# Kernel optimization log

Measured on AMD Instinct MI355X. Metric: run time of the kernel, lower is better.

Reference implementation:

```python
import jax, jax.numpy as jnp
import numpy as np

N_NODES = 500_000
N_EDGES = 16_000_000
C_IN = 1
C_OUT = 4


def gcn_conv(x, edge_index, W, b):
    """PyG GCNConv: add self-loops, symmetric normalization, linear + scatter-add.
    x: [N, Cin], edge_index: [2, E] (src, dst), W: [Cin, Cout], b: [Cout].
    """
    n = x.shape[0]
    loops = jnp.arange(n, dtype=edge_index.dtype)
    src = jnp.concatenate([edge_index[0], loops])  # [E+N]
    dst = jnp.concatenate([edge_index[1], loops])  # [E+N]
    h = x @ W  # [N, Cout]
    # degree at target nodes (with self-loops)
    deg = jax.ops.segment_sum(jnp.ones_like(dst, dtype=h.dtype), dst, num_segments=n)
    dinv = jnp.where(deg > 0, jax.lax.rsqrt(deg), 0.0)  # deg^{-1/2}
    norm = dinv[src] * dinv[dst]  # [E+N]
    msgs = norm[:, None] * h[src]  # [E+N, Cout] gathered + scaled messages
    out = jax.ops.segment_sum(msgs, dst, num_segments=n)  # scatter-add at targets
    return out + b


def setup_inputs() -> dict:
    key = jax.random.key(0)
    k0, k1, k2, k3 = jax.random.split(key, 4)
    x = jax.random.normal(k0, (N_NODES, C_IN), dtype=jnp.float32)
    edge_index = jax.random.randint(k1, (2, N_EDGES), 0, N_NODES, dtype=jnp.int64)
    W1 = jax.random.normal(k2, (C_IN, C_OUT), dtype=jnp.float32) / np.sqrt(C_IN)
    b1 = jnp.zeros((C_OUT,), dtype=jnp.float32)
    W2 = jax.random.normal(k3, (C_OUT, C_OUT), dtype=jnp.float32) / np.sqrt(C_OUT)
    b2 = jnp.zeros((C_OUT,), dtype=jnp.float32)
    return {"x": x, "edge_index": edge_index, "W1": W1, "b1": b1, "W2": W2, "b2": b2}


def reference(x, edge_index, W1, b1, W2, b2):
    h = jax.nn.relu(gcn_conv(x, edge_index, W1, b1))
    return gcn_conv(h, edge_index, W2, b2)
```

## Files before the change

kernel.cpp:

```cpp
#include <hip/hip_runtime.h>


#define B1_BLOCKS 512
#define B1_THREADS 1024
#define TILE1 16384
#define B2_THREADS 1024
#define TILE2 16384
#define MAXNB1 256
#define SORT_STAGE 12032
#define FB_BLOCKS 512
#define FB_THREADS 1024
#define FB_PAD 8
#define MAXNBF 2048


template <int CTRL, int RM, int KOLD>
__device__ __forceinline__ void seg_step1(int m, float& a) {
  const int mm = __builtin_amdgcn_update_dpp(KOLD, m, CTRL, RM, 0xf, true);
  const float f = (mm == m) ? 1.0f : 0.0f;
  const float ba = __int_as_float(
      __builtin_amdgcn_update_dpp(0, __float_as_int(a), CTRL, RM, 0xf, true));
  a = fmaf(ba, f, a);
}

template <int CTRL, int RM, int KOLD>
__device__ __forceinline__ void seg_step4(int m, float& gx, float& gy,
                                          float& gz, float& gw) {
  const int mm = __builtin_amdgcn_update_dpp(KOLD, m, CTRL, RM, 0xf, true);
  const float f = (mm == m) ? 1.0f : 0.0f;
  const float bx = __int_as_float(
      __builtin_amdgcn_update_dpp(0, __float_as_int(gx), CTRL, RM, 0xf, true));
  const float by = __int_as_float(
      __builtin_amdgcn_update_dpp(0, __float_as_int(gy), CTRL, RM, 0xf, true));
  const float bz = __int_as_float(
      __builtin_amdgcn_update_dpp(0, __float_as_int(gz), CTRL, RM, 0xf, true));
  const float bw = __int_as_float(
      __builtin_amdgcn_update_dpp(0, __float_as_int(gw), CTRL, RM, 0xf, true));
  gx = fmaf(bx, f, gx);
  gy = fmaf(by, f, gy);
  gz = fmaf(bz, f, gz);
  gw = fmaf(bw, f, gw);
}

__device__ __forceinline__ void seg_scan1(int m, float& a) {
  seg_step1<0x111, 0xf, 0>(m, a);
  seg_step1<0x112, 0xf, 0>(m, a);
  seg_step1<0x114, 0xf, 0>(m, a);
// ... 70 lines not shown
      int4 d = reinterpret_cast<const int4*>(dt)[k];
      int4 s = reinterpret_cast<const int4*>(st)[k];
      int r0 = atomicAdd(&wcur[d.x >> 11], 1);
      int r1 = atomicAdd(&wcur[d.y >> 11], 1);
      int r2 = atomicAdd(&wcur[d.z >> 11], 1);
      int r3 = atomicAdd(&wcur[d.w >> 11], 1);
      out[r0] = (s.x << 11) | (d.x & 2047);
      out[r1] = (s.y << 11) | (d.y & 2047);
      out[r2] = (s.z << 11) | (d.z & 2047);
      out[r3] = (s.w << 11) | (d.w & 2047);
    }
    for (int k = (nv << 2) + tid; k < tcnt; k += B1_THREADS) {
      int d = dt[k], s = st[k];
      int r = atomicAdd(&wcur[d >> 11], 1);
      out[r] = (s << 11) | (d & 2047);
    }
    __syncthreads();

    const int wv = tid >> 6, lane = tid & 63;
    for (int j = wv; j < nb1; j += 16) {
      const int c = wcur[j] - toff[j];
      if (!c) continue;
      const int gbase = gb[j];
      const long long pbase = (long long)j * C1;
      for (int q = lane; q < c; q += 64) {
        int gi = gbase + q;
        if (gi < C1) pay1[pbase + gi] = out[toff[j] + q];
      }
    }
    __syncthreads();
  }
}

__global__ __launch_bounds__(B2_THREADS) void k_bin2(
    const int* __restrict__ pay1, const int* __restrict__ gcur1, int C1,
    int C2, int* __restrict__ gcur2, int* __restrict__ pay2) {
  __shared__ int out[TILE2];
  __shared__ int hist[8], toff9[9], wcur[8], gb[8];
  const int cb = blockIdx.x >> 1;
  const int half = blockIdx.x & 1;
  const int tid = threadIdx.x;
  const int Lc = min(gcur1[cb], C1);
  int mid = ((Lc >> 1) + 3) & ~3;
  if (mid > Lc) mid = Lc;
  const int h0 = half ? mid : 0;
  const int h1 = half ? Lc : mid;
  const int* seg = pay1 + (long long)cb * C1;

  for (int tb = h0; tb < h1; tb += TILE2) {
    const int tcnt = min(TILE2, h1 - tb);
    const int nv = tcnt >> 2;
    if (tid < 8) hist[tid] = 0;
    __syncthreads();
    const int* pt = seg + tb;

    for (int k = tid; k < nv; k += B2_THREADS) {
      int4 p = reinterpret_cast<const int4*>(pt)[k];
      atomicAdd(&hist[(p.x >> 8) & 7], 1);
      atomicAdd(&hist[(p.y >> 8) & 7], 1);
      atomicAdd(&hist[(p.z >> 8) & 7], 1);
      atomicAdd(&hist[(p.w >> 8) & 7], 1);
    }
    for (int k = (nv << 2) + tid; k < tcnt; k += B2_THREADS)
      atomicAdd(&hist[(pt[k] >> 8) & 7], 1);
    __syncthreads();

    if (tid == 0) {
      int run = 0;
      for (int j = 0; j < 8; ++j) { toff9[j] = run; run += hist[j]; }
      toff9[8] = run;
    }
    __syncthreads();
    if (tid < 8) {
      wcur[tid] = toff9[tid];
      gb[tid] = hist[tid] ? atomicAdd(&gcur2[cb * 8 + tid], hist[tid]) : 0;
    }
    __syncthreads();

    for (int k = tid; k < nv; k += B2_THREADS) {
      int4 p = reinterpret_cast<const int4*>(pt)[k];
      out[atomicAdd(&wcur[(p.x >> 8) & 7], 1)] = ((p.x >> 11) << 8) | (p.x & 255);
      out[atomicAdd(&wcur[(p.y >> 8) & 7], 1)] = ((p.y >> 11) << 8) | (p.y & 255);
      out[atomicAdd(&wcur[(p.z >> 8) & 7], 1)] = ((p.z >> 11) << 8) | (p.z & 255);
      out[atomicAdd(&wcur[(p.w >> 8) & 7], 1)] = ((p.w >> 11) << 8) | (p.w & 255);
    }
    for (int k = (nv << 2) + tid; k < tcnt; k += B2_THREADS) {
      int p = pt[k];
      out[atomicAdd(&wcur[(p >> 8) & 7], 1)] = ((p >> 11) << 8) | (p & 255);
    }
    __syncthreads();

    const int total = toff9[8];
    for (int q = tid; q < total; q += B2_THREADS) {
      int j = (q >= toff9[4]) ? 4 : 0;
      j += (q >= toff9[j + 2]) ? 2 : 0;
      j += (q >= toff9[j + 1]) ? 1 : 0;
      int o = gb[j] + (q - toff9[j]);
      if (o < C2) pay2[(long long)(cb * 8 + j) * C2 + o] = out[q];
    }
    __syncthreads();
  }
}

__global__ __launch_bounds__(FB_THREADS) void k_bin_flat(
    const int* __restrict__ src, const int* __restrict__ dst, int E,
    int chunk, int nbf, int C, int* __restrict__ gcur,
    int* __restrict__ payload) {
  __shared__ int hist[MAXNBF];
  __shared__ int lbase[MAXNBF];
  const int tid = threadIdx.x;
  const long long e0 = (long long)blockIdx.x * chunk;
  long long rem = (long long)E - e0;
  int lim = rem < 0 ? 0 : (rem < chunk ? (int)rem : chunk);
  for (int j = tid; j < nbf; j += FB_THREADS) hist[j] = 0;
  __syncthreads();
  const int* dch = dst + e0;
  const int* sch = src + e0;
  const int nv = lim >> 2;
  for (int k = tid; k < nv; k += FB_THREADS) {
    int4 d = reinterpret_cast<const int4*>(dch)[k];
    atomicAdd(&hist[d.x >> 8], 1);
    atomicAdd(&hist[d.y >> 8], 1);
    atomicAdd(&hist[d.z >> 8], 1);
    atomicAdd(&hist[d.w >> 8], 1);
  }
  for (int k = (nv << 2) + tid; k < lim; k += FB_THREADS)
    atomicAdd(&hist[dch[k] >> 8], 1);
  __syncthreads();
  for (int j = tid; j < nbf; j += FB_THREADS) {
    int c = hist[j];
    lbase[j] = c ? atomicAdd(&gcur[j], (c + FB_PAD - 1) & ~(FB_PAD - 1)) : 0;
    hist[j] = 0;
  }
  __syncthreads();
  for (int k = tid; k < nv; k += FB_THREADS) {
    int4 d = reinterpret_cast<const int4*>(dch)[k];
    int4 s = reinterpret_cast<const int4*>(sch)[k];
    int b0 = d.x >> 8, b1 = d.y >> 8, b2 = d.z >> 8, b3 = d.w >> 8;
    int r0 = atomicAdd(&hist[b0], 1) + lbase[b0];
    int r1 = atomicAdd(&hist[b1], 1) + lbase[b1];
    int r2 = atomicAdd(&hist[b2], 1) + lbase[b2];
    int r3 = atomicAdd(&hist[b3], 1) + lbase[b3];
    if (r0 < C) payload[(long long)b0 * C + r0] = (s.x << 8) | (d.x & 255);
    if (r1 < C) payload[(long long)b1 * C + r1] = (s.y << 8) | (d.y & 255);
    if (r2 < C) payload[(long long)b2 * C + r2] = (s.z << 8) | (d.z & 255);
    if (r3 < C) payload[(long long)b3 * C + r3] = (s.w << 8) | (d.w & 255);
  }
  for (int k = (nv << 2) + tid; k < lim; k += FB_THREADS) {
    int d = dch[k], s = sch[k];
    int bk = d >> 8;
    int r = atomicAdd(&hist[bk], 1) + lbase[bk];
    if (r < C) payload[(long long)bk * C + r] = (s << 8) | (d & 255);
  }
  __syncthreads();
  for (int j = tid; j < nbf; j += FB_THREADS) {
    int c = hist[j];
    if (c) {
      int pc = (c + FB_PAD - 1) & ~(FB_PAD - 1);
      long long base = (long long)j * C;
      for (int k = lbase[j] + c; k < lbase[j] + pc; ++k)
        if (k < C) payload[base + k] = -1;
    }
  }
}

__global__ __launch_bounds__(256) void k_sort(
    int* __restrict__ payload, const int* __restrict__ gcur, int C,
    int n, const float* __restrict__ x,
    int* __restrict__ off_g, float* __restrict__ y) {
  __shared__ int stage[SORT_STAGE];
  __shared__ int hist[256];
  __shared__ int sbuf[2][256];
  __shared__ int cur[256];
  const int b = blockIdx.x, t = threadIdx.x;
  hist[t] = 0;
  __syncthreads();
  int* seg = payload + (long long)b * C;
  const int L = min(gcur[b], C);
  const int nv = L >> 2;
#pragma unroll 2
  for (int k = t; k < nv; k += 256) {
    int4 p = reinterpret_cast<const int4*>(seg)[k];
    reinterpret_cast<int4*>(stage)[k] = p;
    if (p.x >= 0) atomicAdd(&hist[p.x & 255], 1);
    if (p.y >= 0) atomicAdd(&hist[p.y & 255], 1);
    if (p.z >= 0) atomicAdd(&hist[p.z & 255], 1);
    if (p.w >= 0) atomicAdd(&hist[p.w & 255], 1);
  }
  for (int k = (nv << 2) + t; k < L; k += 256) {
    int p = seg[k];
    stage[k] = p;
    if (p >= 0) atomicAdd(&hist[p & 255], 1);
  }
  __syncthreads();
  sbuf[0][t] = hist[t];
  __syncthreads();
  int pi = 0;
  for (int d = 1; d < 256; d <<= 1) {
    int v = sbuf[pi][t];
    if (t >= d) v += sbuf[pi][t - d];
    sbuf[pi ^ 1][t] = v;
    pi ^= 1;
    __syncthreads();
  }
  const int inc = sbuf[pi][t];
  const int exc = inc - hist[t];
  cur[t] = exc;
  off_g[b * 257 + t] = exc;
  if (t == 255) off_g[b * 257 + 256] = inc;
  const int i = (b << 8) + t;
  if (i < n) y[i] = rsqrtf((float)(hist[t] + 1)) * x[i];
  __syncthreads();
#pragma unroll 4
  for (int k = t; k < L; k += 256) {
    int p = stage[k];
    if (p >= 0) {
      int pos = atomicAdd(&cur[p & 255], 1);
      seg[pos] = p;
    }
  }
}

__global__ __launch_bounds__(256) void k_reduce1(
    const int* __restrict__ payload, const int* __restrict__ off_g, int C,
    int n, const float* __restrict__ y, float2* __restrict__ ds) {
  __shared__ float S[256];
  const int b = blockIdx.x, t = threadIdx.x;
  S[t] = 0.0f;
  __syncthreads();
  const int L = off_g[b * 257 + 256];
  const int* seg = payload + (long long)b * C;
  const int lane = t & 63;
  for (int base = t - lane; base < L; base += 256) {
    int k = base + lane;
    bool valid = k < L;
    int p = 0;
    if (valid) p = __builtin_nontemporal_load(seg + k);
    int m = valid ? (p & 255) : 999;
    float v = valid ? y[p >> 8] : 0.0f;
    seg_scan1(m, v);
    int mn = __shfl_down(m, 1, 64);
    if ((lane == 63 || mn != m) && m < 256) atomicAdd(&S[m], v);
  }
  __syncthreads();
  const int i = (b << 8) + t;
  if (i < n) {
    int deg = off_g[b * 257 + t + 1] - off_g[b * 257 + t];
    float r = rsqrtf((float)(deg + 1));
    ds[i] = make_float2(r, r * (S[t] + y[i]));
  }
}

// ... 32 lines not shown
    float gx = r * (h0 * w2[0] + h1 * w2[4] + h2 * w2[8]  + h3 * w2[12]);
    float gy = r * (h0 * w2[1] + h1 * w2[5] + h2 * w2[9]  + h3 * w2[13]);
    float gz = r * (h0 * w2[2] + h1 * w2[6] + h2 * w2[10] + h3 * w2[14]);
    float gw = r * (h0 * w2[3] + h1 * w2[7] + h2 * w2[11] + h3 * w2[15]);
    seg_scan4(m, gx, gy, gz, gw);
    int mn = __shfl_down(m, 1, 64);
    if ((lane == 63 || mn != m) && m < 256) {
      atomicAdd(&S0[m], gx);
      atomicAdd(&S1[m], gy);
      atomicAdd(&S2[m], gz);
      atomicAdd(&S3[m], gw);
    }
  }
  __syncthreads();
  const int i = (b << 8) + t;
  if (i < n) {
    float2 v = ds[i];
    float r = v.x, s = v.y;
    float h0 = fmaxf(fmaf(s, w10, c10), 0.f);
    float h1 = fmaxf(fmaf(s, w11, c11), 0.f);
    float h2 = fmaxf(fmaf(s, w12, c12), 0.f);
    float h3 = fmaxf(fmaf(s, w13, c13), 0.f);
    float gx = r * (h0 * w2[0] + h1 * w2[4] + h2 * w2[8]  + h3 * w2[12]);
    float gy = r * (h0 * w2[1] + h1 * w2[5] + h2 * w2[9]  + h3 * w2[13]);
    float gz = r * (h0 * w2[2] + h1 * w2[6] + h2 * w2[10] + h3 * w2[14]);
    float gw = r * (h0 * w2[3] + h1 * w2[7] + h2 * w2[11] + h3 * w2[15]);
    out[i] = make_float4(b2[0] + r * (S0[t] + gx),
                         b2[1] + r * (S1[t] + gy),
                         b2[2] + r * (S2[t] + gz),
                         b2[3] + r * (S3[t] + gw));
  }
}

extern "C" void kernel_launch(void* const* d_in, const int* in_sizes, int n_in,
                              void* d_out, int out_size, void* d_ws, size_t ws_size,
                              hipStream_t stream) {
  const float* x  = (const float*)d_in[0];
  const int*   ei = (const int*)d_in[1];
  const float* W1 = (const float*)d_in[2];
  const float* b1 = (const float*)d_in[3];
  const float* W2 = (const float*)d_in[4];
  const float* b2 = (const float*)d_in[5];

  const int n = in_sizes[0];
  const int E = in_sizes[1] / 2;
  const int* src = ei;
  const int* dst = ei + E;

  const int nbf = (n + 255) >> 8;
  const int nb1 = (n + 2047) >> 11;
  auto al = [](size_t v) { return (v + 255) & ~(size_t)255; };

  const size_t nn = (size_t)n;
  size_t sz_off = al((size_t)nbf * 257 * 4);
  size_t sz_y   = al(nn * 4);
  size_t sz_ds  = al(nn * 8);
  size_t sz_gc  = al(((size_t)nb1 + nbf) * 4);
  size_t fixed = sz_off + sz_y + sz_ds + sz_gc;

  long long mean1 = (long long)E / (nb1 > 0 ? nb1 : 1);
  long long C1ll = ((mean1 + 2048 + 1024) + 15) & ~15LL;
  long long mean2 = (long long)E / nbf;
  long long C2ll = ((mean2 + 1024) + 15) & ~15LL;
  size_t need_main = fixed + al((size_t)nb1 * C1ll * 4) + al((size_t)nbf * C2ll * 4);
  const bool main_ok = (n <= 524288) && (nb1 <= MAXNB1) && (nbf <= MAXNBF) &&
                       (C2ll <= SORT_STAGE) && (need_main <= ws_size);

  if (main_ok) {
    const int C1 = (int)C1ll, C2 = (int)C2ll;
    char* p = (char*)d_ws;
    int*    pay1  = (int*)p;    p += al((size_t)nb1 * C1 * 4);
    int*    pay2  = (int*)p;    p += al((size_t)nbf * C2 * 4);
    int*    gcur1 = (int*)p;
    int*    gcur2 = gcur1 + nb1;
    p += sz_gc;
    int*    off_g = (int*)p;    p += sz_off;
    float*  y     = (float*)p;  p += sz_y;
    float2* ds    = (float2*)p; p += sz_ds;

    hipMemsetAsync(gcur1, 0, ((size_t)nb1 + nbf) * 4, stream);

    int chunk = (int)(((long long)E + B1_BLOCKS - 1) / B1_BLOCKS);
    chunk = (chunk + 3) & ~3;

    k_bin1<<<B1_BLOCKS, B1_THREADS, 0, stream>>>(src, dst, E, chunk, nb1, C1,
                                                 gcur1, pay1);
    k_bin2<<<nb1 * 2, B2_THREADS, 0, stream>>>(pay1, gcur1, C1, C2, gcur2,
                                               pay2);
    k_sort<<<nbf, 256, 0, stream>>>(pay2, gcur2, C2, n, x, off_g, y);
    k_reduce1<<<nbf, 256, 0, stream>>>(pay2, off_g, C2, n, y, ds);
    k_reduce2<<<nbf, 256, 0, stream>>>(pay2, off_g, C2, n, ds, W1, b1, W2, b2,
                                       (float4*)d_out);
    return;
  }

  {
    double mean = (double)E / nbf;
    long long Cwant = (long long)(mean * 1.10) +
                      (long long)(FB_BLOCKS * FB_PAD / 2) + 512;
    size_t budget = ws_size > fixed ? ws_size - fixed - 4096 : 0;
    long long Cbud = (long long)(budget / ((size_t)nbf * 4));
    long long Cll = Cwant < Cbud ? Cwant : Cbud;
    if (Cll > SORT_STAGE) Cll = SORT_STAGE;
    int C = (int)(Cll & ~(long long)(FB_PAD - 1));

    char* p = (char*)d_ws;
    int*    pay2  = (int*)p;    p += al((size_t)nbf * C * 4);
    int*    gcur  = (int*)p;    p += sz_gc;
    int*    off_g = (int*)p;    p += sz_off;
    float*  y     = (float*)p;  p += sz_y;
    float2* ds    = (float2*)p; p += sz_ds;

    hipMemsetAsync(gcur, 0, (size_t)nbf * 4, stream);

    int chunk = (int)(((long long)E + FB_BLOCKS - 1) / FB_BLOCKS);
    chunk = (chunk + 3) & ~3;

    k_bin_flat<<<FB_BLOCKS, FB_THREADS, 0, stream>>>(src, dst, E, chunk, nbf,
                                                     C, gcur, pay2);
    k_sort<<<nbf, 256, 0, stream>>>(pay2, gcur, C, n, x, off_g, y);
    k_reduce1<<<nbf, 256, 0, stream>>>(pay2, off_g, C, n, y, ds);
    k_reduce2<<<nbf, 256, 0, stream>>>(pay2, off_g, C, n, ds, W1, b1, W2, b2,
                                       (float4*)d_out);
  }
}
```

Measured before the change: 524.0 us.

## Replace second binning pass and sort with LDS-atomic reductions over coarse bins

Removes the second radix binning pass (k_bin2) and the per-fine-bin sort. Three new kernels (degree count, first-layer reduce, second-layer reduce) work directly on the coarse 2048-node buckets with shared-memory atomics, and each reads the whole bucket payload. This drops one full pass that rewrote the edge payload, plus the sort and offset work. In exchange, the reductions depend on LDS float atomics with possible contention, and only nb1 (~245) blocks of 1024 threads run, which may leave the GPU underfilled. Float summation order also becomes nondeterministic.

```diff
diff --git a/kernel.cpp b/kernel.cpp
--- a/kernel.cpp
+++ b/kernel.cpp
@@ -1,18 +1,17 @@
 #include <hip/hip_runtime.h>
 
+
+typedef int iv4 __attribute__((ext_vector_type(4)));
 
 #define B1_BLOCKS 512
 #define B1_THREADS 1024
 #define TILE1 16384
-#define B2_THREADS 1024
-#define TILE2 16384
 #define MAXNB1 256
 #define SORT_STAGE 12032
 #define FB_BLOCKS 512
 #define FB_THREADS 1024
 #define FB_PAD 8
 #define MAXNBF 2048
-
 
 template <int CTRL, int RM, int KOLD>
 __device__ __forceinline__ void seg_step1(int m, float& a) {
@@ -149,73 +148,159 @@
   }
 }
 
-__global__ __launch_bounds__(B2_THREADS) void k_bin2(
+__global__ __launch_bounds__(1024) void k_cnt(
     const int* __restrict__ pay1, const int* __restrict__ gcur1, int C1,
-    int C2, int* __restrict__ gcur2, int* __restrict__ pay2) {
-  __shared__ int out[TILE2];
-  __shared__ int hist[8], toff9[9], wcur[8], gb[8];
-  const int cb = blockIdx.x >> 1;
-  const int half = blockIdx.x & 1;
-  const int tid = threadIdx.x;
-  const int Lc = min(gcur1[cb], C1);
-  int mid = ((Lc >> 1) + 3) & ~3;
-  if (mid > Lc) mid = Lc;
-  const int h0 = half ? mid : 0;
-  const int h1 = half ? Lc : mid;
-  const int* seg = pay1 + (long long)cb * C1;
-
-  for (int tb = h0; tb < h1; tb += TILE2) {
-    const int tcnt = min(TILE2, h1 - tb);
-    const int nv = tcnt >> 2;
-    if (tid < 8) hist[tid] = 0;
-    __syncthreads();
-    const int* pt = seg + tb;
-
-    for (int k = tid; k < nv; k += B2_THREADS) {
-      int4 p = reinterpret_cast<const int4*>(pt)[k];
-      atomicAdd(&hist[(p.x >> 8) & 7], 1);
-      atomicAdd(&hist[(p.y >> 8) & 7], 1);
-      atomicAdd(&hist[(p.z >> 8) & 7], 1);
-      atomicAdd(&hist[(p.w >> 8) & 7], 1);
-    }
-    for (int k = (nv << 2) + tid; k < tcnt; k += B2_THREADS)
-      atomicAdd(&hist[(pt[k] >> 8) & 7], 1);
-    __syncthreads();
-
-    if (tid == 0) {
-      int run = 0;
-      for (int j = 0; j < 8; ++j) { toff9[j] = run; run += hist[j]; }
-      toff9[8] = run;
-    }
-    __syncthreads();
-    if (tid < 8) {
-      wcur[tid] = toff9[tid];
-      gb[tid] = hist[tid] ? atomicAdd(&gcur2[cb * 8 + tid], hist[tid]) : 0;
-    }
-    __syncthreads();
-
-    for (int k = tid; k < nv; k += B2_THREADS) {
-      int4 p = reinterpret_cast<const int4*>(pt)[k];
-      out[atomicAdd(&wcur[(p.x >> 8) & 7], 1)] = ((p.x >> 11) << 8) | (p.x & 255);
-      out[atomicAdd(&wcur[(p.y >> 8) & 7], 1)] = ((p.y >> 11) << 8) | (p.y & 255);
-      out[atomicAdd(&wcur[(p.z >> 8) & 7], 1)] = ((p.z >> 11) << 8) | (p.z & 255);
-      out[atomicAdd(&wcur[(p.w >> 8) & 7], 1)] = ((p.w >> 11) << 8) | (p.w & 255);
-    }
-    for (int k = (nv << 2) + tid; k < tcnt; k += B2_THREADS) {
-      int p = pt[k];
-      out[atomicAdd(&wcur[(p >> 8) & 7], 1)] = ((p >> 11) << 8) | (p & 255);
-    }
-    __syncthreads();
-
-    const int total = toff9[8];
-    for (int q = tid; q < total; q += B2_THREADS) {
-      int j = (q >= toff9[4]) ? 4 : 0;
-      j += (q >= toff9[j + 2]) ? 2 : 0;
-      j += (q >= toff9[j + 1]) ? 1 : 0;
-      int o = gb[j] + (q - toff9[j]);
-      if (o < C2) pay2[(long long)(cb * 8 + j) * C2 + o] = out[q];
-    }
-    __syncthreads();
+    int n, const float* __restrict__ x, int* __restrict__ deg_g,
+    float* __restrict__ y) {
+  __shared__ int hist[2048];
+  const int b = blockIdx.x, t = threadIdx.x;
+  hist[t] = 0;
+  hist[t + 1024] = 0;
+  __syncthreads();
+  const int L = min(gcur1[b], C1);
+  const int* seg = pay1 + (long long)b * C1;
+  const int nv = L >> 2;
+  for (int k = t; k < nv; k += 1024) {
+    iv4 p = __builtin_nontemporal_load(reinterpret_cast<const iv4*>(seg) + k);
+    atomicAdd(&hist[p.x & 2047], 1);
+    atomicAdd(&hist[p.y & 2047], 1);
+    atomicAdd(&hist[p.z & 2047], 1);
+    atomicAdd(&hist[p.w & 2047], 1);
+  }
+  for (int k = (nv << 2) + t; k < L; k += 1024) {
+    int p = __builtin_nontemporal_load(seg + k);
+    atomicAdd(&hist[p & 2047], 1);
+  }
+  __syncthreads();
+  const int base = b << 11;
+#pragma unroll
+  for (int q = 0; q < 2; ++q) {
+    const int sl = t + q * 1024;
+    const int i = base + sl;
+    if (i < n) {
+      const int d = hist[sl];
+      deg_g[i] = d;
+      y[i] = rsqrtf((float)(d + 1)) * x[i];
+    }
+  }
+}
+
+__global__ __launch_bounds__(1024) void k_red1c(
+    const int* __restrict__ pay1, const int* __restrict__ gcur1, int C1,
+    int n, const float* __restrict__ y, const int* __restrict__ deg_g,
+    float2* __restrict__ ds) {
+  __shared__ float S[2048];
+  const int b = blockIdx.x, t = threadIdx.x;
+  S[t] = 0.0f;
+  S[t + 1024] = 0.0f;
+  __syncthreads();
+  const int L = min(gcur1[b], C1);
+  const int* seg = pay1 + (long long)b * C1;
+  const int nv = L >> 2;
+  for (int k = t; k < nv; k += 1024) {
+    iv4 p = __builtin_nontemporal_load(reinterpret_cast<const iv4*>(seg) + k);
+    float vx = y[p.x >> 11];
+    float vy = y[p.y >> 11];
+    float vz = y[p.z >> 11];
+    float vw = y[p.w >> 11];
+    atomicAdd(&S[p.x & 2047], vx);
+    atomicAdd(&S[p.y & 2047], vy);
+    atomicAdd(&S[p.z & 2047], vz);
+    atomicAdd(&S[p.w & 2047], vw);
+  }
+  for (int k = (nv << 2) + t; k < L; k += 1024) {
+    int p = __builtin_nontemporal_load(seg + k);
+    atomicAdd(&S[p & 2047], y[p >> 11]);
+  }
+  __syncthreads();
+  const int base = b << 11;
+#pragma unroll
+  for (int q = 0; q < 2; ++q) {
+    const int sl = t + q * 1024;
+    const int i = base + sl;
+    if (i < n) {
+      const float r = rsqrtf((float)(deg_g[i] + 1));
+      ds[i] = make_float2(r, r * (S[sl] + y[i]));
+    }
+  }
+}
+
+__global__ __launch_bounds__(1024) void k_red2c(
+    const int* __restrict__ pay1, const int* __restrict__ gcur1, int C1,
+    int n, const float2* __restrict__ ds,
+    const float* __restrict__ W1, const float* __restrict__ b1,
+    const float* __restrict__ W2, const float* __restrict__ b2,
+    float4* __restrict__ out) {
+  __shared__ float S0[2048], S1[2048], S2[2048], S3[2048];
+  const int b = blockIdx.x, t = threadIdx.x;
+  S0[t] = 0.f; S0[t + 1024] = 0.f;
+  S1[t] = 0.f; S1[t + 1024] = 0.f;
+  S2[t] = 0.f; S2[t + 1024] = 0.f;
+  S3[t] = 0.f; S3[t + 1024] = 0.f;
+  __syncthreads();
+  const float w10 = W1[0], w11 = W1[1], w12 = W1[2], w13 = W1[3];
+  const float c10 = b1[0], c11 = b1[1], c12 = b1[2], c13 = b1[3];
+  float w2[16];
+#pragma unroll
+  for (int k = 0; k < 16; ++k) w2[k] = W2[k];
+
+  const int L = min(gcur1[b], C1);
+  const int* seg = pay1 + (long long)b * C1;
+  const int nv = L >> 2;
+  for (int k = t; k < nv; k += 1024) {
+    iv4 p4 = __builtin_nontemporal_load(reinterpret_cast<const iv4*>(seg) + k);
+#pragma unroll
+    for (int c = 0; c < 4; ++c) {
+      const int p = (c == 0) ? p4.x : (c == 1) ? p4.y : (c == 2) ? p4.z : p4.w;
+      const int m = p & 2047;
+      const float2 v = ds[p >> 11];
+      const float r = v.x, s = v.y;
+      const float h0 = fmaxf(fmaf(s, w10, c10), 0.f);
+      const float h1 = fmaxf(fmaf(s, w11, c11), 0.f);
+      const float h2 = fmaxf(fmaf(s, w12, c12), 0.f);
+      const float h3 = fmaxf(fmaf(s, w13, c13), 0.f);
+      atomicAdd(&S0[m], r * (h0 * w2[0] + h1 * w2[4] + h2 * w2[8]  + h3 * w2[12]));
+      atomicAdd(&S1[m], r * (h0 * w2[1] + h1 * w2[5] + h2 * w2[9]  + h3 * w2[13]));
+      atomicAdd(&S2[m], r * (h0 * w2[2] + h1 * w2[6] + h2 * w2[10] + h3 * w2[14]));
+      atomicAdd(&S3[m], r * (h0 * w2[3] + h1 * w2[7] + h2 * w2[11] + h3 * w2[15]));
+    }
+  }
+  for (int k = (nv << 2) + t; k < L; k += 1024) {
+    const int p = __builtin_nontemporal_load(seg + k);
+    const int m = p & 2047;
+    const float2 v = ds[p >> 11];
+    const float r = v.x, s = v.y;
+    const float h0 = fmaxf(fmaf(s, w10, c10), 0.f);
+    const float h1 = fmaxf(fmaf(s, w11, c11), 0.f);
+    const float h2 = fmaxf(fmaf(s, w12, c12), 0.f);
+    const float h3 = fmaxf(fmaf(s, w13, c13), 0.f);
+    atomicAdd(&S0[m], r * (h0 * w2[0] + h1 * w2[4] + h2 * w2[8]  + h3 * w2[12]));
+    atomicAdd(&S1[m], r * (h0 * w2[1] + h1 * w2[5] + h2 * w2[9]  + h3 * w2[13]));
+    atomicAdd(&S2[m], r * (h0 * w2[2] + h1 * w2[6] + h2 * w2[10] + h3 * w2[14]));
+    atomicAdd(&S3[m], r * (h0 * w2[3] + h1 * w2[7] + h2 * w2[11] + h3 * w2[15]));
+  }
+  __syncthreads();
+  const int base = b << 11;
+#pragma unroll
+  for (int q = 0; q < 2; ++q) {
+    const int sl = t + q * 1024;
+    const int i = base + sl;
+    if (i < n) {
+      const float2 v = ds[i];
+      const float r = v.x, s = v.y;
+      const float h0 = fmaxf(fmaf(s, w10, c10), 0.f);
+      const float h1 = fmaxf(fmaf(s, w11, c11), 0.f);
+      const float h2 = fmaxf(fmaf(s, w12, c12), 0.f);
+      const float h3 = fmaxf(fmaf(s, w13, c13), 0.f);
+      const float sx = r * (h0 * w2[0] + h1 * w2[4] + h2 * w2[8]  + h3 * w2[12]);
+      const float sy = r * (h0 * w2[1] + h1 * w2[5] + h2 * w2[9]  + h3 * w2[13]);
+      const float sz = r * (h0 * w2[2] + h1 * w2[6] + h2 * w2[10] + h3 * w2[14]);
+      const float sw = r * (h0 * w2[3] + h1 * w2[7] + h2 * w2[11] + h3 * w2[15]);
+      out[i] = make_float4(b2[0] + r * (S0[sl] + sx),
+                           b2[1] + r * (S1[sl] + sy),
+                           b2[2] + r * (S2[sl] + sz),
+                           b2[3] + r * (S3[sl] + sw));
+    }
   }
 }
 
@@ -453,49 +538,44 @@
   auto al = [](size_t v) { return (v + 255) & ~(size_t)255; };
 
   const size_t nn = (size_t)n;
-  size_t sz_off = al((size_t)nbf * 257 * 4);
   size_t sz_y   = al(nn * 4);
+  size_t sz_deg = al(nn * 4);
   size_t sz_ds  = al(nn * 8);
-  size_t sz_gc  = al(((size_t)nb1 + nbf) * 4);
-  size_t fixed = sz_off + sz_y + sz_ds + sz_gc;
 
   long long mean1 = (long long)E / (nb1 > 0 ? nb1 : 1);
-  long long C1ll = ((mean1 + 2048 + 1024) + 15) & ~15LL;
-  long long mean2 = (long long)E / nbf;
-  long long C2ll = ((mean2 + 1024) + 15) & ~15LL;
-  size_t need_main = fixed + al((size_t)nb1 * C1ll * 4) + al((size_t)nbf * C2ll * 4);
-  const bool main_ok = (n <= 524288) && (nb1 <= MAXNB1) && (nbf <= MAXNBF) &&
-                       (C2ll <= SORT_STAGE) && (need_main <= ws_size);
+  long long C1ll = ((mean1 + 3072) + 15) & ~15LL;
+  size_t need_main = al((size_t)nb1 * C1ll * 4) + al((size_t)nb1 * 4) +
+                     sz_y + sz_deg + sz_ds;
+  const bool main_ok = (n <= 524288) && (nb1 <= MAXNB1) &&
+                       (need_main <= ws_size);
 
   if (main_ok) {
-    const int C1 = (int)C1ll, C2 = (int)C2ll;
+    const int C1 = (int)C1ll;
     char* p = (char*)d_ws;
     int*    pay1  = (int*)p;    p += al((size_t)nb1 * C1 * 4);
-    int*    pay2  = (int*)p;    p += al((size_t)nbf * C2 * 4);
-    int*    gcur1 = (int*)p;
-    int*    gcur2 = gcur1 + nb1;
-    p += sz_gc;
-    int*    off_g = (int*)p;    p += sz_off;
+    int*    gcur1 = (int*)p;    p += al((size_t)nb1 * 4);
+    int*    deg_g = (int*)p;    p += sz_deg;
     float*  y     = (float*)p;  p += sz_y;
     float2* ds    = (float2*)p; p += sz_ds;
 
-    hipMemsetAsync(gcur1, 0, ((size_t)nb1 + nbf) * 4, stream);
+    hipMemsetAsync(gcur1, 0, (size_t)nb1 * 4, stream);
 
     int chunk = (int)(((long long)E + B1_BLOCKS - 1) / B1_BLOCKS);
     chunk = (chunk + 3) & ~3;
 
     k_bin1<<<B1_BLOCKS, B1_THREADS, 0, stream>>>(src, dst, E, chunk, nb1, C1,
                                                  gcur1, pay1);
-    k_bin2<<<nb1 * 2, B2_THREADS, 0, stream>>>(pay1, gcur1, C1, C2, gcur2,
-                                               pay2);
-    k_sort<<<nbf, 256, 0, stream>>>(pay2, gcur2, C2, n, x, off_g, y);
-    k_reduce1<<<nbf, 256, 0, stream>>>(pay2, off_g, C2, n, y, ds);
-    k_reduce2<<<nbf, 256, 0, stream>>>(pay2, off_g, C2, n, ds, W1, b1, W2, b2,
-                                       (float4*)d_out);
+    k_cnt<<<nb1, 1024, 0, stream>>>(pay1, gcur1, C1, n, x, deg_g, y);
+    k_red1c<<<nb1, 1024, 0, stream>>>(pay1, gcur1, C1, n, y, deg_g, ds);
+    k_red2c<<<nb1, 1024, 0, stream>>>(pay1, gcur1, C1, n, ds, W1, b1, W2, b2,
+                                      (float4*)d_out);
     return;
   }
 
   {
+    size_t sz_off = al((size_t)nbf * 257 * 4);
+    size_t sz_gc  = al((size_t)nbf * 4);
+    size_t fixed = sz_off + sz_y + sz_ds + sz_gc;
     double mean = (double)E / nbf;
     long long Cwant = (long long)(mean * 1.10) +
                       (long long)(FB_BLOCKS * FB_PAD / 2) + 512;
```

Measured after the change: 677.0 us. 1.29x slower.

## Replace per-bucket sort with degree histogram and shared-atomic unsorted reductions

Applied to the files above, without the earlier changes.

Removes the k_sort pass, which sorted each 256-node bucket by destination. Node degrees are now counted in a shared-memory histogram inside the second binning kernel and flushed with global atomics. A tiny kernel computes y = rsqrt(deg+1)*x, and both reduction passes read the unsorted bucket payload and accumulate into 256-entry shared arrays with atomicAdd. This trades a sort pass and its offset table for shared-memory atomic contention and nondeterministic float summation order. The memset also grows to cover the degree array.

```diff
diff --git a/kernel.cpp b/kernel.cpp
--- a/kernel.cpp
+++ b/kernel.cpp
@@ -12,7 +12,6 @@
 #define FB_THREADS 1024
 #define FB_PAD 8
 #define MAXNBF 2048
-
 
 template <int CTRL, int RM, int KOLD>
 __device__ __forceinline__ void seg_step1(int m, float& a) {
@@ -149,10 +148,12 @@
   }
 }
 
-__global__ __launch_bounds__(B2_THREADS) void k_bin2(
+__global__ __launch_bounds__(B2_THREADS) void k_bin2d(
     const int* __restrict__ pay1, const int* __restrict__ gcur1, int C1,
-    int C2, int* __restrict__ gcur2, int* __restrict__ pay2) {
+    int C2, int* __restrict__ gcur2, int* __restrict__ pay2,
+    int n, int* __restrict__ deg_g) {
   __shared__ int out[TILE2];
+  __shared__ int dh[2048];
   __shared__ int hist[8], toff9[9], wcur[8], gb[8];
   const int cb = blockIdx.x >> 1;
   const int half = blockIdx.x & 1;
@@ -164,6 +165,10 @@
   const int h1 = half ? Lc : mid;
   const int* seg = pay1 + (long long)cb * C1;
 
+  dh[tid] = 0;
+  dh[tid + 1024] = 0;
+  __syncthreads();
+
   for (int tb = h0; tb < h1; tb += TILE2) {
     const int tcnt = min(TILE2, h1 - tb);
     const int nv = tcnt >> 2;
@@ -177,9 +182,16 @@
       atomicAdd(&hist[(p.y >> 8) & 7], 1);
       atomicAdd(&hist[(p.z >> 8) & 7], 1);
       atomicAdd(&hist[(p.w >> 8) & 7], 1);
-    }
-    for (int k = (nv << 2) + tid; k < tcnt; k += B2_THREADS)
-      atomicAdd(&hist[(pt[k] >> 8) & 7], 1);
+      atomicAdd(&dh[p.x & 2047], 1);
+      atomicAdd(&dh[p.y & 2047], 1);
+      atomicAdd(&dh[p.z & 2047], 1);
+      atomicAdd(&dh[p.w & 2047], 1);
+    }
+    for (int k = (nv << 2) + tid; k < tcnt; k += B2_THREADS) {
+      int p = pt[k];
+      atomicAdd(&hist[(p >> 8) & 7], 1);
+      atomicAdd(&dh[p & 2047], 1);
+    }
     __syncthreads();
 
     if (tid == 0) {
@@ -216,6 +228,96 @@
       if (o < C2) pay2[(long long)(cb * 8 + j) * C2 + o] = out[q];
     }
     __syncthreads();
+  }
+
+  const int nbase = cb << 11;
+#pragma unroll
+  for (int q = 0; q < 2; ++q) {
+    const int j = tid + q * 1024;
+    const int c = dh[j];
+    const int i = nbase + j;
+    if (c && i < n) atomicAdd(&deg_g[i], c);
+  }
+}
+
+__global__ __launch_bounds__(256) void k_y(
+    int n, const int* __restrict__ deg_g, const float* __restrict__ x,
+    float* __restrict__ y) {
+  const int i = blockIdx.x * 256 + threadIdx.x;
+  if (i < n) y[i] = rsqrtf((float)(deg_g[i] + 1)) * x[i];
+}
+
+__global__ __launch_bounds__(256) void k_red1u(
+    const int* __restrict__ pay2, const int* __restrict__ gcur2, int C2,
+    int n, const float* __restrict__ y, const int* __restrict__ deg_g,
+    float2* __restrict__ ds) {
+  __shared__ float S[256];
+  const int b = blockIdx.x, t = threadIdx.x;
+  S[t] = 0.0f;
+  __syncthreads();
+  const int L = min(gcur2[b], C2);
+  const int* seg = pay2 + (long long)b * C2;
+  for (int k = t; k < L; k += 256) {
+    const int p = __builtin_nontemporal_load(seg + k);
+    atomicAdd(&S[p & 255], y[p >> 8]);
+  }
+  __syncthreads();
+  const int i = (b << 8) + t;
+  if (i < n) {
+    const float r = rsqrtf((float)(deg_g[i] + 1));
+    ds[i] = make_float2(r, r * (S[t] + y[i]));
+  }
+}
+
+__global__ __launch_bounds__(256) void k_red2u(
+    const int* __restrict__ pay2, const int* __restrict__ gcur2, int C2,
+    int n, const float2* __restrict__ ds,
+    const float* __restrict__ W1, const float* __restrict__ b1,
+    const float* __restrict__ W2, const float* __restrict__ b2,
+    float4* __restrict__ out) {
+  __shared__ float S0[256], S1[256], S2[256], S3[256];
+  const int b = blockIdx.x, t = threadIdx.x;
+  S0[t] = 0.f; S1[t] = 0.f; S2[t] = 0.f; S3[t] = 0.f;
+  __syncthreads();
+  const float w10 = W1[0], w11 = W1[1], w12 = W1[2], w13 = W1[3];
+  const float c10 = b1[0], c11 = b1[1], c12 = b1[2], c13 = b1[3];
+  float w2[16];
+#pragma unroll
+  for (int k = 0; k < 16; ++k) w2[k] = W2[k];
+
+  const int L = min(gcur2[b], C2);
+  const int* seg = pay2 + (long long)b * C2;
+  for (int k = t; k < L; k += 256) {
+    const int p = __builtin_nontemporal_load(seg + k);
+    const int m = p & 255;
+    const float2 v = ds[p >> 8];
+    const float r = v.x, s = v.y;
+    const float h0 = fmaxf(fmaf(s, w10, c10), 0.f);
+    const float h1 = fmaxf(fmaf(s, w11, c11), 0.f);
+    const float h2 = fmaxf(fmaf(s, w12, c12), 0.f);
+    const float h3 = fmaxf(fmaf(s, w13, c13), 0.f);
+    atomicAdd(&S0[m], r * (h0 * w2[0] + h1 * w2[4] + h2 * w2[8]  + h3 * w2[12]));
+    atomicAdd(&S1[m], r * (h0 * w2[1] + h1 * w2[5] + h2 * w2[9]  + h3 * w2[13]));
+    atomicAdd(&S2[m], r * (h0 * w2[2] + h1 * w2[6] + h2 * w2[10] + h3 * w2[14]));
+    atomicAdd(&S3[m], r * (h0 * w2[3] + h1 * w2[7] + h2 * w2[11] + h3 * w2[15]));
+  }
+  __syncthreads();
+  const int i = (b << 8) + t;
+  if (i < n) {
+    const float2 v = ds[i];
+    const float r = v.x, s = v.y;
+    const float h0 = fmaxf(fmaf(s, w10, c10), 0.f);
+    const float h1 = fmaxf(fmaf(s, w11, c11), 0.f);
+    const float h2 = fmaxf(fmaf(s, w12, c12), 0.f);
+    const float h3 = fmaxf(fmaf(s, w13, c13), 0.f);
+    const float sx = r * (h0 * w2[0] + h1 * w2[4] + h2 * w2[8]  + h3 * w2[12]);
+    const float sy = r * (h0 * w2[1] + h1 * w2[5] + h2 * w2[9]  + h3 * w2[13]);
+    const float sz = r * (h0 * w2[2] + h1 * w2[6] + h2 * w2[10] + h3 * w2[14]);
+    const float sw = r * (h0 * w2[3] + h1 * w2[7] + h2 * w2[11] + h3 * w2[15]);
+    out[i] = make_float4(b2[0] + r * (S0[t] + sx),
+                         b2[1] + r * (S1[t] + sy),
+                         b2[2] + r * (S2[t] + sz),
+                         b2[3] + r * (S3[t] + sw));
   }
 }
 
@@ -453,19 +555,18 @@
   auto al = [](size_t v) { return (v + 255) & ~(size_t)255; };
 
   const size_t nn = (size_t)n;
-  size_t sz_off = al((size_t)nbf * 257 * 4);
   size_t sz_y   = al(nn * 4);
   size_t sz_ds  = al(nn * 8);
-  size_t sz_gc  = al(((size_t)nb1 + nbf) * 4);
-  size_t fixed = sz_off + sz_y + sz_ds + sz_gc;
 
   long long mean1 = (long long)E / (nb1 > 0 ? nb1 : 1);
   long long C1ll = ((mean1 + 2048 + 1024) + 15) & ~15LL;
-  long long mean2 = (long long)E / nbf;
+  long long mean2 = (long long)E / (nbf > 0 ? nbf : 1);
   long long C2ll = ((mean2 + 1024) + 15) & ~15LL;
-  size_t need_main = fixed + al((size_t)nb1 * C1ll * 4) + al((size_t)nbf * C2ll * 4);
-  const bool main_ok = (n <= 524288) && (nb1 <= MAXNB1) && (nbf <= MAXNBF) &&
-                       (C2ll <= SORT_STAGE) && (need_main <= ws_size);
+  size_t sz_zero = al(((size_t)nb1 + nbf + nn) * 4);
+  size_t need_main = al((size_t)nb1 * C1ll * 4) + al((size_t)nbf * C2ll * 4) +
+                     sz_zero + sz_y + sz_ds;
+  const bool main_ok = (n <= 524288) && (nb1 <= MAXNB1) &&
+                       (need_main <= ws_size);
 
   if (main_ok) {
     const int C1 = (int)C1ll, C2 = (int)C2ll;
@@ -474,28 +575,31 @@
     int*    pay2  = (int*)p;    p += al((size_t)nbf * C2 * 4);
     int*    gcur1 = (int*)p;
     int*    gcur2 = gcur1 + nb1;
-    p += sz_gc;
-    int*    off_g = (int*)p;    p += sz_off;
+    int*    deg_g = gcur2 + nbf;
+    p += sz_zero;
     float*  y     = (float*)p;  p += sz_y;
     float2* ds    = (float2*)p; p += sz_ds;
 
-    hipMemsetAsync(gcur1, 0, ((size_t)nb1 + nbf) * 4, stream);
+    hipMemsetAsync(gcur1, 0, ((size_t)nb1 + nbf + nn) * 4, stream);
 
     int chunk = (int)(((long long)E + B1_BLOCKS - 1) / B1_BLOCKS);
     chunk = (chunk + 3) & ~3;
 
     k_bin1<<<B1_BLOCKS, B1_THREADS, 0, stream>>>(src, dst, E, chunk, nb1, C1,
                                                  gcur1, pay1);
-    k_bin2<<<nb1 * 2, B2_THREADS, 0, stream>>>(pay1, gcur1, C1, C2, gcur2,
-                                               pay2);
-    k_sort<<<nbf, 256, 0, stream>>>(pay2, gcur2, C2, n, x, off_g, y);
-    k_reduce1<<<nbf, 256, 0, stream>>>(pay2, off_g, C2, n, y, ds);
-    k_reduce2<<<nbf, 256, 0, stream>>>(pay2, off_g, C2, n, ds, W1, b1, W2, b2,
-                                       (float4*)d_out);
+    k_bin2d<<<nb1 * 2, B2_THREADS, 0, stream>>>(pay1, gcur1, C1, C2, gcur2,
+                                                pay2, n, deg_g);
+    k_y<<<(n + 255) / 256, 256, 0, stream>>>(n, deg_g, x, y);
+    k_red1u<<<nbf, 256, 0, stream>>>(pay2, gcur2, C2, n, y, deg_g, ds);
+    k_red2u<<<nbf, 256, 0, stream>>>(pay2, gcur2, C2, n, ds, W1, b1, W2, b2,
+                                     (float4*)d_out);
     return;
   }
 
   {
+    size_t sz_off = al((size_t)nbf * 257 * 4);
+    size_t sz_gc  = al((size_t)nbf * 4);
+    size_t fixed = sz_off + sz_y + sz_ds + sz_gc;
     double mean = (double)E / nbf;
     long long Cwant = (long long)(mean * 1.10) +
                       (long long)(FB_BLOCKS * FB_PAD / 2) + 512;
```

Measured after the change: 705.2 us. +34.6%, slower.

## Fuse second binning pass and per-bucket sort into one counting-sort kernel

Applied to the files above, without the earlier changes.

Replaces the k_bin2 (split coarse buckets into 8 sub-buckets) and k_sort (in-place 256-way counting sort per fine bucket) kernels with a single k_csort kernel. Each 1024-thread block takes one coarse bucket of 2048 nodes, builds a 2048-entry histogram in shared memory, prefix-scans it, writes the degree-based y and the off_g offsets, then scatters entries directly into their final sorted positions in pay2. This removes one full read/write pass over the edge payload and one kernel launch, along with the gcur2 counters. In exchange the final scatter goes to global memory through 2048 shared atomic cursors with less locality, and only 256 large blocks run, which may limit occupancy.

```diff
diff --git a/kernel.cpp b/kernel.cpp
--- a/kernel.cpp
+++ b/kernel.cpp
@@ -4,15 +4,12 @@
 #define B1_BLOCKS 512
 #define B1_THREADS 1024
 #define TILE1 16384
-#define B2_THREADS 1024
-#define TILE2 16384
 #define MAXNB1 256
 #define SORT_STAGE 12032
 #define FB_BLOCKS 512
 #define FB_THREADS 1024
 #define FB_PAD 8
 #define MAXNBF 2048
-
 
 template <int CTRL, int RM, int KOLD>
 __device__ __forceinline__ void seg_step1(int m, float& a) {
@@ -149,192 +146,78 @@
   }
 }
 
-__global__ __launch_bounds__(B2_THREADS) void k_bin2(
+__global__ __launch_bounds__(1024) void k_csort(
     const int* __restrict__ pay1, const int* __restrict__ gcur1, int C1,
-    int C2, int* __restrict__ gcur2, int* __restrict__ pay2) {
-  __shared__ int out[TILE2];
-  __shared__ int hist[8], toff9[9], wcur[8], gb[8];
-  const int cb = blockIdx.x >> 1;
-  const int half = blockIdx.x & 1;
-  const int tid = threadIdx.x;
-  const int Lc = min(gcur1[cb], C1);
-  int mid = ((Lc >> 1) + 3) & ~3;
-  if (mid > Lc) mid = Lc;
-  const int h0 = half ? mid : 0;
-  const int h1 = half ? Lc : mid;
-  const int* seg = pay1 + (long long)cb * C1;
-
-  for (int tb = h0; tb < h1; tb += TILE2) {
-    const int tcnt = min(TILE2, h1 - tb);
-    const int nv = tcnt >> 2;
-    if (tid < 8) hist[tid] = 0;
-    __syncthreads();
-    const int* pt = seg + tb;
-
-    for (int k = tid; k < nv; k += B2_THREADS) {
-      int4 p = reinterpret_cast<const int4*>(pt)[k];
-      atomicAdd(&hist[(p.x >> 8) & 7], 1);
-      atomicAdd(&hist[(p.y >> 8) & 7], 1);
-      atomicAdd(&hist[(p.z >> 8) & 7], 1);
-      atomicAdd(&hist[(p.w >> 8) & 7], 1);
-    }
-    for (int k = (nv << 2) + tid; k < tcnt; k += B2_THREADS)
-      atomicAdd(&hist[(pt[k] >> 8) & 7], 1);
-    __syncthreads();
-
-    if (tid == 0) {
-      int run = 0;
-      for (int j = 0; j < 8; ++j) { toff9[j] = run; run += hist[j]; }
-      toff9[8] = run;
-    }
-    __syncthreads();
-    if (tid < 8) {
-      wcur[tid] = toff9[tid];
-      gb[tid] = hist[tid] ? atomicAdd(&gcur2[cb * 8 + tid], hist[tid]) : 0;
-    }
-    __syncthreads();
-
-    for (int k = tid; k < nv; k += B2_THREADS) {
-      int4 p = reinterpret_cast<const int4*>(pt)[k];
-      out[atomicAdd(&wcur[(p.x >> 8) & 7], 1)] = ((p.x >> 11) << 8) | (p.x & 255);
-      out[atomicAdd(&wcur[(p.y >> 8) & 7], 1)] = ((p.y >> 11) << 8) | (p.y & 255);
-      out[atomicAdd(&wcur[(p.z >> 8) & 7], 1)] = ((p.z >> 11) << 8) | (p.z & 255);
-      out[atomicAdd(&wcur[(p.w >> 8) & 7], 1)] = ((p.w >> 11) << 8) | (p.w & 255);
-    }
-    for (int k = (nv << 2) + tid; k < tcnt; k += B2_THREADS) {
-      int p = pt[k];
-      out[atomicAdd(&wcur[(p >> 8) & 7], 1)] = ((p >> 11) << 8) | (p & 255);
-    }
-    __syncthreads();
-
-    const int total = toff9[8];
-    for (int q = tid; q < total; q += B2_THREADS) {
-      int j = (q >= toff9[4]) ? 4 : 0;
-      j += (q >= toff9[j + 2]) ? 2 : 0;
-      j += (q >= toff9[j + 1]) ? 1 : 0;
-      int o = gb[j] + (q - toff9[j]);
-      if (o < C2) pay2[(long long)(cb * 8 + j) * C2 + o] = out[q];
-    }
-    __syncthreads();
-  }
-}
-
-__global__ __launch_bounds__(FB_THREADS) void k_bin_flat(
-    const int* __restrict__ src, const int* __restrict__ dst, int E,
-    int chunk, int nbf, int C, int* __restrict__ gcur,
-    int* __restrict__ payload) {
-  __shared__ int hist[MAXNBF];
-  __shared__ int lbase[MAXNBF];
-  const int tid = threadIdx.x;
-  const long long e0 = (long long)blockIdx.x * chunk;
-  long long rem = (long long)E - e0;
-  int lim = rem < 0 ? 0 : (rem < chunk ? (int)rem : chunk);
-  for (int j = tid; j < nbf; j += FB_THREADS) hist[j] = 0;
-  __syncthreads();
-  const int* dch = dst + e0;
-  const int* sch = src + e0;
-  const int nv = lim >> 2;
-  for (int k = tid; k < nv; k += FB_THREADS) {
-    int4 d = reinterpret_cast<const int4*>(dch)[k];
-    atomicAdd(&hist[d.x >> 8], 1);
-    atomicAdd(&hist[d.y >> 8], 1);
-    atomicAdd(&hist[d.z >> 8], 1);
-    atomicAdd(&hist[d.w >> 8], 1);
-  }
-  for (int k = (nv << 2) + tid; k < lim; k += FB_THREADS)
-    atomicAdd(&hist[dch[k] >> 8], 1);
-  __syncthreads();
-  for (int j = tid; j < nbf; j += FB_THREADS) {
-    int c = hist[j];
-    lbase[j] = c ? atomicAdd(&gcur[j], (c + FB_PAD - 1) & ~(FB_PAD - 1)) : 0;
-    hist[j] = 0;
-  }
-  __syncthreads();
-  for (int k = tid; k < nv; k += FB_THREADS) {
-    int4 d = reinterpret_cast<const int4*>(dch)[k];
-    int4 s = reinterpret_cast<const int4*>(sch)[k];
-    int b0 = d.x >> 8, b1 = d.y >> 8, b2 = d.z >> 8, b3 = d.w >> 8;
-    int r0 = atomicAdd(&hist[b0], 1) + lbase[b0];
-    int r1 = atomicAdd(&hist[b1], 1) + lbase[b1];
-    int r2 = atomicAdd(&hist[b2], 1) + lbase[b2];
-    int r3 = atomicAdd(&hist[b3], 1) + lbase[b3];
-    if (r0 < C) payload[(long long)b0 * C + r0] = (s.x << 8) | (d.x & 255);
-    if (r1 < C) payload[(long long)b1 * C + r1] = (s.y << 8) | (d.y & 255);
-    if (r2 < C) payload[(long long)b2 * C + r2] = (s.z << 8) | (d.z & 255);
-    if (r3 < C) payload[(long long)b3 * C + r3] = (s.w << 8) | (d.w & 255);
-  }
-  for (int k = (nv << 2) + tid; k < lim; k += FB_THREADS) {
-    int d = dch[k], s = sch[k];
-    int bk = d >> 8;
-    int r = atomicAdd(&hist[bk], 1) + lbase[bk];
-    if (r < C) payload[(long long)bk * C + r] = (s << 8) | (d & 255);
-  }
-  __syncthreads();
-  for (int j = tid; j < nbf; j += FB_THREADS) {
-    int c = hist[j];
-    if (c) {
-      int pc = (c + FB_PAD - 1) & ~(FB_PAD - 1);
-      long long base = (long long)j * C;
-      for (int k = lbase[j] + c; k < lbase[j] + pc; ++k)
-        if (k < C) payload[base + k] = -1;
-    }
-  }
-}
-
-__global__ __launch_bounds__(256) void k_sort(
-    int* __restrict__ payload, const int* __restrict__ gcur, int C,
-    int n, const float* __restrict__ x,
-    int* __restrict__ off_g, float* __restrict__ y) {
-  __shared__ int stage[SORT_STAGE];
-  __shared__ int hist[256];
-  __shared__ int sbuf[2][256];
-  __shared__ int cur[256];
+    int C2, int n, const float* __restrict__ x,
+    int* __restrict__ off_g, float* __restrict__ y,
+    int* __restrict__ pay2) {
+  __shared__ int dh[2048];
+  __shared__ int off2[2048];
+  __shared__ int sb[2][1024];
   const int b = blockIdx.x, t = threadIdx.x;
-  hist[t] = 0;
-  __syncthreads();
-  int* seg = payload + (long long)b * C;
-  const int L = min(gcur[b], C);
+  const int L = min(gcur1[b], C1);
+  const int* seg = pay1 + (long long)b * C1;
+  dh[t] = 0;
+  dh[t + 1024] = 0;
+  __syncthreads();
+
   const int nv = L >> 2;
-#pragma unroll 2
-  for (int k = t; k < nv; k += 256) {
+  for (int k = t; k < nv; k += 1024) {
     int4 p = reinterpret_cast<const int4*>(seg)[k];
-    reinterpret_cast<int4*>(stage)[k] = p;
-    if (p.x >= 0) atomicAdd(&hist[p.x & 255], 1);
-    if (p.y >= 0) atomicAdd(&hist[p.y & 255], 1);
-    if (p.z >= 0) atomicAdd(&hist[p.z & 255], 1);
-    if (p.w >= 0) atomicAdd(&hist[p.w & 255], 1);
-  }
-  for (int k = (nv << 2) + t; k < L; k += 256) {
-    int p = seg[k];
-    stage[k] = p;
-    if (p >= 0) atomicAdd(&hist[p & 255], 1);
-  }
-  __syncthreads();
-  sbuf[0][t] = hist[t];
-  __syncthreads();
-  int pi = 0;
-  for (int d = 1; d < 256; d <<= 1) {
-    int v = sbuf[pi][t];
-    if (t >= d) v += sbuf[pi][t - d];
-    sbuf[pi ^ 1][t] = v;
-    pi ^= 1;
-    __syncthreads();
-  }
-  const int inc = sbuf[pi][t];
-  const int exc = inc - hist[t];
-  cur[t] = exc;
-  off_g[b * 257 + t] = exc;
-  if (t == 255) off_g[b * 257 + 256] = inc;
-  const int i = (b << 8) + t;
-  if (i < n) y[i] = rsqrtf((float)(hist[t] + 1)) * x[i];
-  __syncthreads();
-#pragma unroll 4
-  for (int k = t; k < L; k += 256) {
-    int p = stage[k];
-    if (p >= 0) {
-      int pos = atomicAdd(&cur[p & 255], 1);
-      seg[pos] = p;
-    }
+    atomicAdd(&dh[p.x & 2047], 1);
+    atomicAdd(&dh[p.y & 2047], 1);
+    atomicAdd(&dh[p.z & 2047], 1);
+    atomicAdd(&dh[p.w & 2047], 1);
+  }
+  for (int k = (nv << 2) + t; k < L; k += 1024)
+    atomicAdd(&dh[seg[k] & 2047], 1);
+  __syncthreads();
+
+#pragma unroll
+  for (int r = 0; r < 2; ++r) {
+    const int base = r << 10;
+    const int c0 = dh[base + t];
+    sb[0][t] = c0;
+    __syncthreads();
+    int pi = 0;
+    for (int d = 1; d < 256; d <<= 1) {
+      int v = sb[pi][t];
+      if ((t & 255) >= d) v += sb[pi][t - d];
+      sb[pi ^ 1][t] = v;
+      pi ^= 1;
+      __syncthreads();
+    }
+    const int inc = sb[pi][t];
+    const int exc = inc - c0;
+    off2[base + t] = exc;
+    const int f = (b << 3) + ((base + t) >> 8);
+    const int tt = t & 255;
+    off_g[f * 257 + tt] = min(exc, C2);
+    if (tt == 255) off_g[f * 257 + 256] = min(inc, C2);
+    const int i = (b << 11) + base + t;
+    if (i < n) y[i] = rsqrtf((float)(c0 + 1)) * x[i];
+    __syncthreads();
+  }
+
+  for (int k = t; k < nv; k += 1024) {
+    int4 p = reinterpret_cast<const int4*>(seg)[k];
+#pragma unroll
+    for (int c = 0; c < 4; ++c) {
+      const int pv = (c == 0) ? p.x : (c == 1) ? p.y : (c == 2) ? p.z : p.w;
+      const int j = pv & 2047;
+      const int pos = atomicAdd(&off2[j], 1);
+      if (pos < C2)
+        pay2[(long long)((b << 3) + (j >> 8)) * C2 + pos] =
+            ((pv >> 11) << 8) | (j & 255);
+    }
+  }
+  for (int k = (nv << 2) + t; k < L; k += 1024) {
+    const int pv = seg[k];
+    const int j = pv & 2047;
+    const int pos = atomicAdd(&off2[j], 1);
+    if (pos < C2)
+      pay2[(long long)((b << 3) + (j >> 8)) * C2 + pos] =
+          ((pv >> 11) << 8) | (j & 255);
   }
 }
 
@@ -433,6 +316,125 @@
   }
 }
 
+__global__ __launch_bounds__(FB_THREADS) void k_bin_flat(
+    const int* __restrict__ src, const int* __restrict__ dst, int E,
+    int chunk, int nbf, int C, int* __restrict__ gcur,
+    int* __restrict__ payload) {
+  __shared__ int hist[MAXNBF];
+  __shared__ int lbase[MAXNBF];
+  const int tid = threadIdx.x;
+  const long long e0 = (long long)blockIdx.x * chunk;
+  long long rem = (long long)E - e0;
+  int lim = rem < 0 ? 0 : (rem < chunk ? (int)rem : chunk);
+  for (int j = tid; j < nbf; j += FB_THREADS) hist[j] = 0;
+  __syncthreads();
+  const int* dch = dst + e0;
+  const int* sch = src + e0;
+  const int nv = lim >> 2;
+  for (int k = tid; k < nv; k += FB_THREADS) {
+    int4 d = reinterpret_cast<const int4*>(dch)[k];
+    atomicAdd(&hist[d.x >> 8], 1);
+    atomicAdd(&hist[d.y >> 8], 1);
+    atomicAdd(&hist[d.z >> 8], 1);
+    atomicAdd(&hist[d.w >> 8], 1);
+  }
+  for (int k = (nv << 2) + tid; k < lim; k += FB_THREADS)
+    atomicAdd(&hist[dch[k] >> 8], 1);
+  __syncthreads();
+  for (int j = tid; j < nbf; j += FB_THREADS) {
+    int c = hist[j];
+    lbase[j] = c ? atomicAdd(&gcur[j], (c + FB_PAD - 1) & ~(FB_PAD - 1)) : 0;
+    hist[j] = 0;
+  }
+  __syncthreads();
+  for (int k = tid; k < nv; k += FB_THREADS) {
+    int4 d = reinterpret_cast<const int4*>(dch)[k];
+    int4 s = reinterpret_cast<const int4*>(sch)[k];
+    int b0 = d.x >> 8, b1 = d.y >> 8, b2 = d.z >> 8, b3 = d.w >> 8;
+    int r0 = atomicAdd(&hist[b0], 1) + lbase[b0];
+    int r1 = atomicAdd(&hist[b1], 1) + lbase[b1];
+    int r2 = atomicAdd(&hist[b2], 1) + lbase[b2];
+    int r3 = atomicAdd(&hist[b3], 1) + lbase[b3];
+    if (r0 < C) payload[(long long)b0 * C + r0] = (s.x << 8) | (d.x & 255);
+    if (r1 < C) payload[(long long)b1 * C + r1] = (s.y << 8) | (d.y & 255);
+    if (r2 < C) payload[(long long)b2 * C + r2] = (s.z << 8) | (d.z & 255);
+    if (r3 < C) payload[(long long)b3 * C + r3] = (s.w << 8) | (d.w & 255);
+  }
+  for (int k = (nv << 2) + tid; k < lim; k += FB_THREADS) {
+    int d = dch[k], s = sch[k];
+    int bk = d >> 8;
+    int r = atomicAdd(&hist[bk], 1) + lbase[bk];
+    if (r < C) payload[(long long)bk * C + r] = (s << 8) | (d & 255);
+  }
+  __syncthreads();
+  for (int j = tid; j < nbf; j += FB_THREADS) {
+    int c = hist[j];
+    if (c) {
+      int pc = (c + FB_PAD - 1) & ~(FB_PAD - 1);
+      long long base = (long long)j * C;
+      for (int k = lbase[j] + c; k < lbase[j] + pc; ++k)
+        if (k < C) payload[base + k] = -1;
+    }
+  }
+}
+
+__global__ __launch_bounds__(256) void k_sort(
+    int* __restrict__ payload, const int* __restrict__ gcur, int C,
+    int n, const float* __restrict__ x,
+    int* __restrict__ off_g, float* __restrict__ y) {
+  __shared__ int stage[SORT_STAGE];
+  __shared__ int hist[256];
+  __shared__ int sbuf[2][256];
+  __shared__ int cur[256];
+  const int b = blockIdx.x, t = threadIdx.x;
+  hist[t] = 0;
+  __syncthreads();
+  int* seg = payload + (long long)b * C;
+  const int L = min(gcur[b], C);
+  const int nv = L >> 2;
+#pragma unroll 2
+  for (int k = t; k < nv; k += 256) {
+    int4 p = reinterpret_cast<const int4*>(seg)[k];
+    reinterpret_cast<int4*>(stage)[k] = p;
+    if (p.x >= 0) atomicAdd(&hist[p.x & 255], 1);
+    if (p.y >= 0) atomicAdd(&hist[p.y & 255], 1);
+    if (p.z >= 0) atomicAdd(&hist[p.z & 255], 1);
+    if (p.w >= 0) atomicAdd(&hist[p.w & 255], 1);
+  }
+  for (int k = (nv << 2) + t; k < L; k += 256) {
+    int p = seg[k];
+    stage[k] = p;
+    if (p >= 0) atomicAdd(&hist[p & 255], 1);
+  }
+  __syncthreads();
+  sbuf[0][t] = hist[t];
+  __syncthreads();
+  int pi = 0;
+  for (int d = 1; d < 256; d <<= 1) {
+    int v = sbuf[pi][t];
+    if (t >= d) v += sbuf[pi][t - d];
+    sbuf[pi ^ 1][t] = v;
+    pi ^= 1;
+    __syncthreads();
+  }
+  const int inc = sbuf[pi][t];
+  const int exc = inc - hist[t];
+  cur[t] = exc;
+  off_g[b * 257 + t] = exc;
+  if (t == 255) off_g[b * 257 + 256] = inc;
+  const int i = (b << 8) + t;
+  if (i < n) y[i] = rsqrtf((float)(hist[t] + 1)) * x[i];
+  __syncthreads();
+#pragma unroll 4
+  for (int k = t; k < L; k += 256) {
+    int p = stage[k];
+    if (p >= 0) {
+      int pos = atomicAdd(&cur[p & 255], 1);
+      seg[pos] = p;
+    }
+  }
+}
+
 extern "C" void kernel_launch(void* const* d_in, const int* in_sizes, int n_in,
                               void* d_out, int out_size, void* d_ws, size_t ws_size,
                               hipStream_t stream) {
@@ -456,39 +458,35 @@
   size_t sz_off = al((size_t)nbf * 257 * 4);
   size_t sz_y   = al(nn * 4);
   size_t sz_ds  = al(nn * 8);
-  size_t sz_gc  = al(((size_t)nb1 + nbf) * 4);
-  size_t fixed = sz_off + sz_y + sz_ds + sz_gc;
 
   long long mean1 = (long long)E / (nb1 > 0 ? nb1 : 1);
   long long C1ll = ((mean1 + 2048 + 1024) + 15) & ~15LL;
-  long long mean2 = (long long)E / nbf;
+  long long mean2 = (long long)E / (nbf > 0 ? nbf : 1);
   long long C2ll = ((mean2 + 1024) + 15) & ~15LL;
-  size_t need_main = fixed + al((size_t)nb1 * C1ll * 4) + al((size_t)nbf * C2ll * 4);
-  const bool main_ok = (n <= 524288) && (nb1 <= MAXNB1) && (nbf <= MAXNBF) &&
-                       (C2ll <= SORT_STAGE) && (need_main <= ws_size);
+  size_t need_main = al((size_t)nb1 * C1ll * 4) + al((size_t)nbf * C2ll * 4) +
+                     al((size_t)nb1 * 4) + sz_off + sz_y + sz_ds;
+  const bool main_ok = (n <= 524288) && (nb1 <= MAXNB1) &&
+                       ((nb1 << 3) >= nbf) && (need_main <= ws_size);
 
   if (main_ok) {
     const int C1 = (int)C1ll, C2 = (int)C2ll;
     char* p = (char*)d_ws;
     int*    pay1  = (int*)p;    p += al((size_t)nb1 * C1 * 4);
     int*    pay2  = (int*)p;    p += al((size_t)nbf * C2 * 4);
-    int*    gcur1 = (int*)p;
-    int*    gcur2 = gcur1 + nb1;
-    p += sz_gc;
+    int*    gcur1 = (int*)p;    p += al((size_t)nb1 * 4);
     int*    off_g = (int*)p;    p += sz_off;
     float*  y     = (float*)p;  p += sz_y;
     float2* ds    = (float2*)p; p += sz_ds;
 
-    hipMemsetAsync(gcur1, 0, ((size_t)nb1 + nbf) * 4, stream);
+    hipMemsetAsync(gcur1, 0, (size_t)nb1 * 4, stream);
 
     int chunk = (int)(((long long)E + B1_BLOCKS - 1) / B1_BLOCKS);
     chunk = (chunk + 3) & ~3;
 
     k_bin1<<<B1_BLOCKS, B1_THREADS, 0, stream>>>(src, dst, E, chunk, nb1, C1,
                                                  gcur1, pay1);
-    k_bin2<<<nb1 * 2, B2_THREADS, 0, stream>>>(pay1, gcur1, C1, C2, gcur2,
-                                               pay2);
-    k_sort<<<nbf, 256, 0, stream>>>(pay2, gcur2, C2, n, x, off_g, y);
+    k_csort<<<nb1, 1024, 0, stream>>>(pay1, gcur1, C1, C2, n, x, off_g, y,
+                                      pay2);
     k_reduce1<<<nbf, 256, 0, stream>>>(pay2, off_g, C2, n, y, ds);
     k_reduce2<<<nbf, 256, 0, stream>>>(pay2, off_g, C2, n, ds, W1, b1, W2, b2,
                                        (float4*)d_out);
@@ -496,6 +494,8 @@
   }
 
   {
+    size_t sz_gc  = al((size_t)nbf * 4);
+    size_t fixed = sz_off + sz_y + sz_ds + sz_gc;
     double mean = (double)E / nbf;
     long long Cwant = (long long)(mean * 1.10) +
                       (long long)(FB_BLOCKS * FB_PAD / 2) + 512;
```

New measurement: 594.5 us. +13.4%, slower.
